# Kernel optimization log

Measured on AMD Instinct MI355X. Metric: run time of the kernel, lower is better.

The kernel has to match this reference:

```python
import jax, jax.numpy as jnp
import numpy as np

EPS = 1e-5  # BatchNorm2d default eps
HEAD_DIM = 64


def conv1x1_bn_silu(x, w, gamma, beta, mean, var):
    # x: [B, Cin, H, W], w: [Cout, Cin] (1x1 conv, no bias)
    y = jnp.einsum('oc,bchw->bohw', w, x)
    scale = (gamma / jnp.sqrt(var + EPS))[None, :, None, None]
    shift = (beta - mean * gamma / jnp.sqrt(var + EPS))[None, :, None, None]
    y = y * scale + shift
    return y * jax.nn.sigmoid(y)  # SiLU


def setup_inputs() -> dict:
    key = jax.random.key(0)
    ks = jax.random.split(key, 11)
    B, C, H, W = 4, 256, 64, 64
    C3 = 3 * C
    return {
        'x': jax.random.normal(ks[0], (B, C, H, W), jnp.float32),
        'qkv_w': jax.random.normal(ks[1], (C3, C), jnp.float32) * (1.0 / np.sqrt(C)),
        'qkv_gamma': jax.random.uniform(ks[2], (C3,), jnp.float32, 0.5, 1.5),
        'qkv_beta': jax.random.normal(ks[3], (C3,), jnp.float32) * 0.1,
        'qkv_mean': jax.random.normal(ks[4], (C3,), jnp.float32) * 0.1,
        'qkv_var': jax.random.uniform(ks[5], (C3,), jnp.float32, 0.5, 1.5),
        'proj_w': jax.random.normal(ks[6], (C, C), jnp.float32) * (1.0 / np.sqrt(C)),
        'proj_gamma': jax.random.uniform(ks[7], (C,), jnp.float32, 0.5, 1.5),
        'proj_beta': jax.random.normal(ks[8], (C,), jnp.float32) * 0.1,
        'proj_mean': jax.random.normal(ks[9], (C,), jnp.float32) * 0.1,
        'proj_var': jax.random.uniform(ks[10], (C,), jnp.float32, 0.5, 1.5),
    }


def reference(x, qkv_w, qkv_gamma, qkv_beta, qkv_mean, qkv_var,
              proj_w, proj_gamma, proj_beta, proj_mean, proj_var):
    B, C, H, W = x.shape
    hd = HEAD_DIM
    nh = C // hd
    scale = hd ** -0.5

    qkv = conv1x1_bn_silu(x, qkv_w, qkv_gamma, qkv_beta, qkv_mean, qkv_var)
    # [B, 3C, H, W] -> [B, 3, nh, hd, HW] -> (3, B, nh, HW, hd)
    qkv = qkv.reshape(B, 3, nh, hd, H * W).transpose(1, 0, 2, 4, 3)
    q, k, v = qkv[0], qkv[1], qkv[2]  # each [B, nh, HW, hd]

    attn = jnp.einsum('bhqd,bhkd->bhqk', q, k) * scale
    attn = jax.nn.softmax(attn, axis=-1)
    out = jnp.einsum('bhqk,bhkd->bhqd', attn, v)  # [B, nh, HW, hd]
    out = out.transpose(0, 1, 3, 2).reshape(B, C, H, W)

    return conv1x1_bn_silu(out, proj_w, proj_gamma, proj_beta, proj_mean, proj_var)
```

## Files before the change

kernel.cpp:

```cpp
#include <hip/hip_runtime.h>
#include <hip/hip_bf16.h>
#include <math.h>

#define SLEN 4096
#define CIN 256
#define C3 768
#define NH 4
#define HD 64
#define BATCH 4

typedef __attribute__((ext_vector_type(8))) short bf16x8;
typedef __attribute__((ext_vector_type(4))) float f32x4;
typedef __attribute__((ext_vector_type(16))) float f32x16;

typedef const __attribute__((address_space(1))) void GVoid;
typedef __attribute__((address_space(3))) void LVoid;

__device__ __forceinline__ void gl2lds16(const void* g, void* l) {
    __builtin_amdgcn_global_load_lds((GVoid*)g, (LVoid*)l, 16, 0, 0);
}

__device__ __forceinline__ short f2bf(float f) {
    union { float f; unsigned u; } v; v.f = f;
    unsigned r = v.u + 0x7fff + ((v.u >> 16) & 1);
    return (short)(r >> 16);
}

__device__ __forceinline__ unsigned cvt_pk(float lo, float hi) {
    unsigned r;
    asm("v_cvt_pk_bf16_f32 %0, %1, %2" : "=v"(r) : "v"(lo), "v"(hi));
    return r;
}

__global__ void k_convert_w(const float* __restrict__ qkvw, const float* __restrict__ projw,
                            short* __restrict__ qkvw_bf, short* __restrict__ projw_bf) {
    int i = blockIdx.x * 256 + threadIdx.x;
    if (i < C3 * CIN) qkvw_bf[i] = f2bf(qkvw[i]);
    if (i < CIN * CIN) projw_bf[i] = f2bf(projw[i]);
}

__global__ void k_transpose_x(const float* __restrict__ x, short* __restrict__ xT) {
    __shared__ float t[32][33];
    int b = blockIdx.z;
    int c0 = blockIdx.y * 32, s0 = blockIdx.x * 32;
    int tid = threadIdx.x;
    int r = tid >> 3, c4 = (tid & 7) * 4;
    const float* src = x + ((size_t)b * CIN + c0 + r) * SLEN + s0 + c4;
    float4 v = *reinterpret_cast<const float4*>(src);
    t[r][c4 + 0] = v.x; t[r][c4 + 1] = v.y; t[r][c4 + 2] = v.z; t[r][c4 + 3] = v.w;
    __syncthreads();
    int s_r = tid >> 3, cc = (tid & 7) * 4;
    short4 o = make_short4(f2bf(t[cc + 0][s_r]), f2bf(t[cc + 1][s_r]),
                           f2bf(t[cc + 2][s_r]), f2bf(t[cc + 3][s_r]));
    *reinterpret_cast<short4*>(xT + ((size_t)b * SLEN + s0 + s_r) * CIN + c0 + cc) = o;
}

__launch_bounds__(256)
__global__ void k_qkv(const short* __restrict__ xT, const short* __restrict__ wbf,
                      const float* __restrict__ g, const float* __restrict__ be,
                      const float* __restrict__ mu, const float* __restrict__ va,
                      short* __restrict__ Q, short* __restrict__ Kb, short* __restrict__ Vt) {
    int wv = threadIdx.x >> 6, l = threadIdx.x & 63, lr = l & 15, lg = l >> 4;
    int b = blockIdx.z;
    int s0 = blockIdx.x * 128 + wv * 32;
    int o0 = blockIdx.y * 64;
    f32x4 acc[2][4] = {};
    const short* aptr = xT + ((size_t)b * SLEN + s0 + lr) * CIN + lg * 8;
    const short* bptr = wbf + (size_t)(o0 + lr) * CIN + lg * 8;
#pragma unroll
    for (int k0 = 0; k0 < CIN; k0 += 32) {
        bf16x8 a0 = *(const bf16x8*)(aptr + k0);
        bf16x8 a1 = *(const bf16x8*)(aptr + 16 * CIN + k0);
#pragma unroll
        for (int oj = 0; oj < 4; oj++) {
            bf16x8 bb = *(const bf16x8*)(bptr + oj * 16 * CIN + k0);
            acc[0][oj] = __builtin_amdgcn_mfma_f32_16x16x32_bf16(a0, bb, acc[0][oj], 0, 0, 0);
            acc[1][oj] = __builtin_amdgcn_mfma_f32_16x16x32_bf16(a1, bb, acc[1][oj], 0, 0, 0);
        }
    }
    int which = o0 >> 8;
    int h = (o0 & 255) >> 6;
    int bh = b * NH + h;
    const float QSC = 0.125f * 1.44269504088896f;
#pragma unroll
    for (int oj = 0; oj < 4; oj++) {
        int o = o0 + oj * 16 + lr;
        float sc = g[o] * rsqrtf(va[o] + 1e-5f);
        float sh = be[o] - mu[o] * sc;
        int d = o & 63;
#pragma unroll
        for (int qi = 0; qi < 2; qi++) {
#pragma unroll
            for (int i = 0; i < 4; i++) {
                float y = acc[qi][oj][i] * sc + sh;
                float z = y / (1.f + __expf(-y));
                int s = s0 + qi * 16 + lg * 4 + i;
                if (which == 0) {
                    Q[((size_t)bh * SLEN + s) * HD + d] = f2bf(z * QSC);
                } else if (which == 1) {
                    Kb[((size_t)bh * SLEN + s) * HD + d] = f2bf(z);
                } else {
                    Vt[((size_t)bh * HD + d) * SLEN + s] = f2bf(z);
                }
            }
        }
    }
}

__launch_bounds__(256, 2)
__global__ void k_attn(const short* __restrict__ Q, const short* __restrict__ Kg,
                       const short* __restrict__ Vg, short* __restrict__ aout) {
    __shared__ __align__(16) char lds[16384 + 32768];
    int tid = threadIdx.x;
    int wv = tid >> 6, l = tid & 63;
    int q32 = l & 31;
    int hi  = l >> 5;

    int bid = blockIdx.x;
    int xcd = bid & 7, slot = bid >> 3;
    int bh = 2 * xcd + (slot & 1);
    int q0 = (slot >> 1) * 128 + wv * 32;

    const short* kg = Kg + (size_t)bh * SLEN * HD;
    const short* vg = Vg + (size_t)bh * HD * SLEN;

    bf16x8 qf[4];
    {
        const short* qb = Q + ((size_t)bh * SLEN + q0 + q32) * HD + hi * 8;
        qf[0] = *(const bf16x8*)(qb);
        qf[1] = *(const bf16x8*)(qb + 16);
        qf[2] = *(const bf16x8*)(qb + 32);
        qf[3] = *(const bf16x8*)(qb + 48);
    }

    bf16x8 ones;
#pragma unroll
    for (int e = 0; e < 8; ++e) ones[e] = (short)0x3F80;

    f32x16 oacc0 = {}, oacc1 = {}, sacc = {};
    float mrun = 0.0f, bA = 0.0f, bB = 0.0f;

    int colsw = (((l & 7) ^ (l >> 3)) << 4);
    const char* kgB = (const char*)kg;
    const char* vgB = (const char*)vg;
    int ksrc = (wv * 16 + (l >> 3)) * 128 + colsw;
    int vsrc = (wv * 16 + (l >> 3)) * 8192 + colsw;
    int wdst = wv * 2048;

#define STAGE(T, KB, VB) do { \
    gl2lds16(kgB + (size_t)(T) * 8192 + ksrc,          lds + (KB) * 8192 + wdst); \
    gl2lds16(kgB + (size_t)(T) * 8192 + ksrc + 1024,   lds + (KB) * 8192 + wdst + 1024); \
    gl2lds16(vgB + (size_t)(T) * 128 + vsrc,           lds + 16384 + (VB) * 8192 + wdst); \
    gl2lds16(vgB + (size_t)(T) * 128 + vsrc + 65536,   lds + 16384 + (VB) * 8192 + wdst + 1024); \
} while (0)

#define VMBAR() do { \
    asm volatile("s_waitcnt vmcnt(0) lgkmcnt(0)" ::: "memory"); \
    __builtin_amdgcn_s_barrier(); \
    asm volatile("" ::: "memory"); \
} while (0)

    int swz = (l & 7) << 4;
    int a0 = q32 * 128 + ((0 * 32 + hi * 16) ^ swz);
    int a1 = q32 * 128 + ((1 * 32 + hi * 16) ^ swz);
    int a2 = q32 * 128 + ((2 * 32 + hi * 16) ^ swz);
    int a3 = q32 * 128 + ((3 * 32 + hi * 16) ^ swz);

#define QKT(KB, D0, D1, BSET) do { \
    BSET = mrun; \
    float nb_ = -mrun; \
    _Pragma("unroll") for (int r_ = 0; r_ < 16; ++r_) { D0[r_] = nb_; D1[r_] = nb_; } \
    __builtin_amdgcn_s_setprio(1); \
    { \
        bf16x8 k0_, k1_; \
        k0_ = *(const bf16x8*)(lds + a0 + (KB) * 8192); \
        k1_ = *(const bf16x8*)(lds + a0 + (KB) * 8192 + 4096); \
        D0 = __builtin_amdgcn_mfma_f32_32x32x16_bf16(k0_, qf[0], D0, 0, 0, 0); \
        D1 = __builtin_amdgcn_mfma_f32_32x32x16_bf16(k1_, qf[0], D1, 0, 0, 0); \
        k0_ = *(const bf16x8*)(lds + a1 + (KB) * 8192); \
        k1_ = *(const bf16x8*)(lds + a1 + (KB) * 8192 + 4096); \
        D0 = __builtin_amdgcn_mfma_f32_32x32x16_bf16(k0_, qf[1], D0, 0, 0, 0); \
        D1 = __builtin_amdgcn_mfma_f32_32x32x16_bf16(k1_, qf[1], D1, 0, 0, 0); \
        k0_ = *(const bf16x8*)(lds + a2 + (KB) * 8192); \
        k1_ = *(const bf16x8*)(lds + a2 + (KB) * 8192 + 4096); \
        D0 = __builtin_amdgcn_mfma_f32_32x32x16_bf16(k0_, qf[2], D0, 0, 0, 0); \
        D1 = __builtin_amdgcn_mfma_f32_32x32x16_bf16(k1_, qf[2], D1, 0, 0, 0); \
        k0_ = *(const bf16x8*)(lds + a3 + (KB) * 8192); \
        k1_ = *(const bf16x8*)(lds + a3 + (KB) * 8192 + 4096); \
        D0 = __builtin_amdgcn_mfma_f32_32x32x16_bf16(k0_, qf[3], D0, 0, 0, 0); \
        D1 = __builtin_amdgcn_mfma_f32_32x32x16_bf16(k1_, qf[3], D1, 0, 0, 0); \
    } \
    __builtin_amdgcn_s_setprio(0); \
} while (0)

#define PVKC(AK, SV, BASE, VB) do { \
    unsigned A0_ = cvt_pk(SV[(BASE) + 0], SV[(BASE) + 1]); \
    unsigned A1_ = cvt_pk(SV[(BASE) + 2], SV[(BASE) + 3]); \
    unsigned A2_ = cvt_pk(SV[(BASE) + 4], SV[(BASE) + 5]); \
    unsigned A3_ = cvt_pk(SV[(BASE) + 6], SV[(BASE) + 7]); \
    asm volatile("v_permlane32_swap_b32 %0, %1" : "+v"(A0_), "+v"(A2_)); \
    asm volatile("v_permlane32_swap_b32 %0, %1" : "+v"(A1_), "+v"(A3_)); \
    union { bf16x8 v; unsigned u[4]; } pf_; \
    pf_.u[0] = A0_; pf_.u[1] = A1_; pf_.u[2] = A2_; pf_.u[3] = A3_; \
    bf16x8 v0_ = *(const bf16x8*)(lds + (AK) + 16384 + (VB) * 8192); \
    bf16x8 v1_ = *(const bf16x8*)(lds + (AK) + 16384 + (VB) * 8192 + 4096); \
    oacc0 = __builtin_amdgcn_mfma_f32_32x32x16_bf16(v0_, pf_.v, oacc0, 0, 0, 0); \
    oacc1 = __builtin_amdgcn_mfma_f32_32x32x16_bf16(v1_, pf_.v, oacc1, 0, 0, 0); \
    sacc  = __builtin_amdgcn_mfma_f32_32x32x16_bf16(ones, pf_.v, sacc, 0, 0, 0); \
} while (0)

#define SMPV(VB, S0, S1, BSET) do { \
    float pa_ = S0[0], pb_ = S0[8], pc_ = S1[0], pd_ = S1[8]; \
    _Pragma("unroll") for (int r_ = 1; r_ < 8; ++r_) { \
        pa_ = fmaxf(pa_, S0[r_]); pb_ = fmaxf(pb_, S0[8 + r_]); \
        pc_ = fmaxf(pc_, S1[r_]); pd_ = fmaxf(pd_, S1[8 + r_]); \
    } \
    float pms_ = fmaxf(fmaxf(pa_, pb_), fmaxf(pc_, pd_)); \
    float c1_ = pms_, c2_ = pms_; \
    asm volatile("" : "+v"(c2_));  \
    asm volatile("v_permlane32_swap_b32 %0, %1" : "+v"(c1_), "+v"(c2_)); \
    pms_ = fmaxf(c1_, c2_); \
    float db_ = mrun - (BSET); \
    if (!__all(pms_ <= db_ + 10.0f)) { \
        float mn_ = fmaxf(mrun, pms_ + (BSET)); \
        float al_ = __builtin_amdgcn_exp2f(mrun - mn_); \
        _Pragma("unroll") for (int r_ = 0; r_ < 16; ++r_) { oacc0[r_] *= al_; oacc1[r_] *= al_; } \
        sacc[0] *= al_; \
        mrun = mn_; db_ = mn_ - (BSET); \
    } \
    if (__all(db_ == 0.0f)) { \
        _Pragma("unroll") for (int r_ = 0; r_ < 16; ++r_) { \
            S0[r_] = __builtin_amdgcn_exp2f(S0[r_]); \
            S1[r_] = __builtin_amdgcn_exp2f(S1[r_]); \
        } \
    } else { \
        _Pragma("unroll") for (int r_ = 0; r_ < 16; ++r_) { \
            S0[r_] = __builtin_amdgcn_exp2f(S0[r_] - db_); \
            S1[r_] = __builtin_amdgcn_exp2f(S1[r_] - db_); \
        } \
    } \
    __builtin_amdgcn_s_setprio(1); \
    PVKC(a0, S0, 0, VB); \
    PVKC(a1, S0, 8, VB); \
    PVKC(a2, S1, 0, VB); \
    PVKC(a3, S1, 8, VB); \
    __builtin_amdgcn_s_setprio(0); \
} while (0)

    f32x16 sA0, sA1, sB0, sB1;

    STAGE(0, 0, 0);
    VMBAR();
    STAGE(1, 1, 1);
    QKT(0, sA0, sA1, bA);
    VMBAR();

    for (int j = 0; j < 15; ++j) {
        STAGE(4 * j + 2, 0, 2); QKT(1, sB0, sB1, bB); SMPV(0, sA0, sA1, bA); VMBAR();
        STAGE(4 * j + 3, 1, 3); QKT(0, sA0, sA1, bA); SMPV(1, sB0, sB1, bB); VMBAR();
        STAGE(4 * j + 4, 0, 0); QKT(1, sB0, sB1, bB); SMPV(2, sA0, sA1, bA); VMBAR();
        STAGE(4 * j + 5, 1, 1); QKT(0, sA0, sA1, bA); SMPV(3, sB0, sB1, bB); VMBAR();
    }
    STAGE(62, 0, 2); QKT(1, sB0, sB1, bB); SMPV(0, sA0, sA1, bA); VMBAR();
    STAGE(63, 1, 3); QKT(0, sA0, sA1, bA); SMPV(1, sB0, sB1, bB); VMBAR();
    QKT(1, sB0, sB1, bB); SMPV(2, sA0, sA1, bA);
    SMPV(3, sB0, sB1, bB);

    float inv = 1.f / sacc[0];
    int b = bh >> 2, h = bh & 3;
    short* ob = aout + ((size_t)b * SLEN + q0 + q32) * CIN + h * HD;
#pragma unroll
    for (int g4 = 0; g4 < 4; ++g4) {
        uint2 st0, st1;
        st0.x = cvt_pk(oacc0[4 * g4 + 0] * inv, oacc0[4 * g4 + 1] * inv);
        st0.y = cvt_pk(oacc0[4 * g4 + 2] * inv, oacc0[4 * g4 + 3] * inv);
        st1.x = cvt_pk(oacc1[4 * g4 + 0] * inv, oacc1[4 * g4 + 1] * inv);
        st1.y = cvt_pk(oacc1[4 * g4 + 2] * inv, oacc1[4 * g4 + 3] * inv);
        *(uint2*)(ob + 8 * g4 + 4 * hi) = st0;
        *(uint2*)(ob + 32 + 8 * g4 + 4 * hi) = st1;
    }
#undef STAGE
#undef VMBAR
#undef QKT
#undef PVKC
#undef SMPV
}

__launch_bounds__(256)
__global__ void k_proj(const short* __restrict__ aout, const short* __restrict__ wbf,
                       const float* __restrict__ g, const float* __restrict__ be,
                       const float* __restrict__ mu, const float* __restrict__ va,
                       float* __restrict__ out) {
    int wv = threadIdx.x >> 6, l = threadIdx.x & 63, lr = l & 15, lg = l >> 4;
    int b = blockIdx.z;
    int s0 = blockIdx.x * 128 + wv * 32;
    int o0 = blockIdx.y * 64;
    f32x4 acc[2][4] = {};
    const short* aptr = aout + ((size_t)b * SLEN + s0 + lr) * CIN + lg * 8;
    const short* bptr = wbf + (size_t)(o0 + lr) * CIN + lg * 8;
#pragma unroll
    for (int k0 = 0; k0 < CIN; k0 += 32) {
        bf16x8 a0 = *(const bf16x8*)(aptr + k0);
        bf16x8 a1 = *(const bf16x8*)(aptr + 16 * CIN + k0);
#pragma unroll
        for (int oj = 0; oj < 4; oj++) {
            bf16x8 bb = *(const bf16x8*)(bptr + oj * 16 * CIN + k0);
            acc[0][oj] = __builtin_amdgcn_mfma_f32_16x16x32_bf16(a0, bb, acc[0][oj], 0, 0, 0);
            acc[1][oj] = __builtin_amdgcn_mfma_f32_16x16x32_bf16(a1, bb, acc[1][oj], 0, 0, 0);
        }
    }
#pragma unroll
    for (int oj = 0; oj < 4; oj++) {
        int o = o0 + oj * 16 + lr;
        float sc = g[o] * rsqrtf(va[o] + 1e-5f);
        float sh = be[o] - mu[o] * sc;
#pragma unroll
        for (int qi = 0; qi < 2; qi++) {
            float4 st;
            float* stp = &st.x;
#pragma unroll
            for (int i = 0; i < 4; i++) {
                float y = acc[qi][oj][i] * sc + sh;
                stp[i] = y / (1.f + __expf(-y));
            }
            int s = s0 + qi * 16 + lg * 4;
            *reinterpret_cast<float4*>(out + ((size_t)b * CIN + o) * SLEN + s) = st;
        }
    }
}

extern "C" void kernel_launch(void* const* d_in, const int* in_sizes, int n_in,
                              void* d_out, int out_size, void* d_ws, size_t ws_size,
                              hipStream_t stream) {
    const float* x    = (const float*)d_in[0];
    const float* qkvw = (const float*)d_in[1];
    const float* qg   = (const float*)d_in[2];
    const float* qbe  = (const float*)d_in[3];
    const float* qmu  = (const float*)d_in[4];
    const float* qva  = (const float*)d_in[5];
    const float* pw   = (const float*)d_in[6];
    const float* pg   = (const float*)d_in[7];
    const float* pbe  = (const float*)d_in[8];
    const float* pmu  = (const float*)d_in[9];
    const float* pva  = (const float*)d_in[10];
    float* out = (float*)d_out;

    char* ws = (char*)d_ws;
    short* xT       = (short*)(ws);
    short* qkvw_bf  = (short*)(ws + 8388608);
    short* projw_bf = (short*)(ws + 8781824);
    short* Qb       = (short*)(ws + 8912896);
    short* Kb       = (short*)(ws + 17301504);
    short* Vt       = (short*)(ws + 25690112);
    short* aout     = (short*)(ws + 34078720);

    k_convert_w<<<768, 256, 0, stream>>>(qkvw, pw, qkvw_bf, projw_bf);
    k_transpose_x<<<dim3(128, 8, 4), 256, 0, stream>>>(x, xT);
    k_qkv<<<dim3(32, 12, 4), 256, 0, stream>>>(xT, qkvw_bf, qg, qbe, qmu, qva, Qb, Kb, Vt);
    k_attn<<<512, 256, 0, stream>>>(Qb, Kb, Vt, aout);
    k_proj<<<dim3(32, 4, 4), 256, 0, stream>>>(aout, projw_bf, pg, pbe, pmu, pva, out);
}
```

Measured before the change: 159.7 us.

## Process two 32-row query tiles per wave to reuse K/V LDS loads

```diff
diff --git a/kernel.cpp b/kernel.cpp
--- a/kernel.cpp
+++ b/kernel.cpp
@@ -107,7 +107,7 @@
     }
 }
 
-__launch_bounds__(256, 2)
+__launch_bounds__(256, 1)
 __global__ void k_attn(const short* __restrict__ Q, const short* __restrict__ Kg,
                        const short* __restrict__ Vg, short* __restrict__ aout) {
     __shared__ __align__(16) char lds[16384 + 32768];
@@ -119,26 +119,31 @@
     int bid = blockIdx.x;
     int xcd = bid & 7, slot = bid >> 3;
     int bh = 2 * xcd + (slot & 1);
-    int q0 = (slot >> 1) * 128 + wv * 32;
+    int q0 = (slot >> 1) * 256 + wv * 64;
 
     const short* kg = Kg + (size_t)bh * SLEN * HD;
     const short* vg = Vg + (size_t)bh * HD * SLEN;
 
-    bf16x8 qf[4];
+    bf16x8 qfL[4], qfR[4];
     {
         const short* qb = Q + ((size_t)bh * SLEN + q0 + q32) * HD + hi * 8;
-        qf[0] = *(const bf16x8*)(qb);
-        qf[1] = *(const bf16x8*)(qb + 16);
-        qf[2] = *(const bf16x8*)(qb + 32);
-        qf[3] = *(const bf16x8*)(qb + 48);
+        qfL[0] = *(const bf16x8*)(qb);
+        qfL[1] = *(const bf16x8*)(qb + 16);
+        qfL[2] = *(const bf16x8*)(qb + 32);
+        qfL[3] = *(const bf16x8*)(qb + 48);
+        const short* qb2 = qb + 32 * HD;
+        qfR[0] = *(const bf16x8*)(qb2);
+        qfR[1] = *(const bf16x8*)(qb2 + 16);
+        qfR[2] = *(const bf16x8*)(qb2 + 32);
+        qfR[3] = *(const bf16x8*)(qb2 + 48);
     }
 
     bf16x8 ones;
 #pragma unroll
     for (int e = 0; e < 8; ++e) ones[e] = (short)0x3F80;
 
-    f32x16 oacc0 = {}, oacc1 = {}, sacc = {};
-    float mrun = 0.0f, bA = 0.0f, bB = 0.0f;
+    f32x16 oaccL0 = {}, oaccL1 = {}, oaccR0 = {}, oaccR1 = {}, saccL = {}, saccR = {};
+    float mrunL = 0.0f, mrunR = 0.0f, bAL = 0.0f, bAR = 0.0f, bBL = 0.0f, bBR = 0.0f;
 
     int colsw = (((l & 7) ^ (l >> 3)) << 4);
     const char* kgB = (const char*)kg;
@@ -166,124 +171,158 @@
     int a2 = q32 * 128 + ((2 * 32 + hi * 16) ^ swz);
     int a3 = q32 * 128 + ((3 * 32 + hi * 16) ^ swz);
 
-#define QKT(KB, D0, D1, BSET) do { \
-    BSET = mrun; \
-    float nb_ = -mrun; \
-    _Pragma("unroll") for (int r_ = 0; r_ < 16; ++r_) { D0[r_] = nb_; D1[r_] = nb_; } \
+#define MM(A, B, C) __builtin_amdgcn_mfma_f32_32x32x16_bf16(A, B, C, 0, 0, 0)
+
+#define QKT2(KB, DL0, DL1, DR0, DR1, BL, BR) do { \
+    BL = mrunL; BR = mrunR; \
+    float nbl_ = -mrunL, nbr_ = -mrunR; \
+    _Pragma("unroll") for (int r_ = 0; r_ < 16; ++r_) { \
+        DL0[r_] = nbl_; DL1[r_] = nbl_; DR0[r_] = nbr_; DR1[r_] = nbr_; } \
     __builtin_amdgcn_s_setprio(1); \
     { \
         bf16x8 k0_, k1_; \
         k0_ = *(const bf16x8*)(lds + a0 + (KB) * 8192); \
         k1_ = *(const bf16x8*)(lds + a0 + (KB) * 8192 + 4096); \
-        D0 = __builtin_amdgcn_mfma_f32_32x32x16_bf16(k0_, qf[0], D0, 0, 0, 0); \
-        D1 = __builtin_amdgcn_mfma_f32_32x32x16_bf16(k1_, qf[0], D1, 0, 0, 0); \
+        DL0 = MM(k0_, qfL[0], DL0); DL1 = MM(k1_, qfL[0], DL1); \
+        DR0 = MM(k0_, qfR[0], DR0); DR1 = MM(k1_, qfR[0], DR1); \
         k0_ = *(const bf16x8*)(lds + a1 + (KB) * 8192); \
         k1_ = *(const bf16x8*)(lds + a1 + (KB) * 8192 + 4096); \
-        D0 = __builtin_amdgcn_mfma_f32_32x32x16_bf16(k0_, qf[1], D0, 0, 0, 0); \
-        D1 = __builtin_amdgcn_mfma_f32_32x32x16_bf16(k1_, qf[1], D1, 0, 0, 0); \
+        DL0 = MM(k0_, qfL[1], DL0); DL1 = MM(k1_, qfL[1], DL1); \
+        DR0 = MM(k0_, qfR[1], DR0); DR1 = MM(k1_, qfR[1], DR1); \
         k0_ = *(const bf16x8*)(lds + a2 + (KB) * 8192); \
         k1_ = *(const bf16x8*)(lds + a2 + (KB) * 8192 + 4096); \
-        D0 = __builtin_amdgcn_mfma_f32_32x32x16_bf16(k0_, qf[2], D0, 0, 0, 0); \
-        D1 = __builtin_amdgcn_mfma_f32_32x32x16_bf16(k1_, qf[2], D1, 0, 0, 0); \
+        DL0 = MM(k0_, qfL[2], DL0); DL1 = MM(k1_, qfL[2], DL1); \
+        DR0 = MM(k0_, qfR[2], DR0); DR1 = MM(k1_, qfR[2], DR1); \
         k0_ = *(const bf16x8*)(lds + a3 + (KB) * 8192); \
         k1_ = *(const bf16x8*)(lds + a3 + (KB) * 8192 + 4096); \
-        D0 = __builtin_amdgcn_mfma_f32_32x32x16_bf16(k0_, qf[3], D0, 0, 0, 0); \
-        D1 = __builtin_amdgcn_mfma_f32_32x32x16_bf16(k1_, qf[3], D1, 0, 0, 0); \
+        DL0 = MM(k0_, qfL[3], DL0); DL1 = MM(k1_, qfL[3], DL1); \
+        DR0 = MM(k0_, qfR[3], DR0); DR1 = MM(k1_, qfR[3], DR1); \
     } \
     __builtin_amdgcn_s_setprio(0); \
 } while (0)
 
-#define PVKC(AK, SV, BASE, VB) do { \
-    unsigned A0_ = cvt_pk(SV[(BASE) + 0], SV[(BASE) + 1]); \
-    unsigned A1_ = cvt_pk(SV[(BASE) + 2], SV[(BASE) + 3]); \
-    unsigned A2_ = cvt_pk(SV[(BASE) + 4], SV[(BASE) + 5]); \
-    unsigned A3_ = cvt_pk(SV[(BASE) + 6], SV[(BASE) + 7]); \
-    asm volatile("v_permlane32_swap_b32 %0, %1" : "+v"(A0_), "+v"(A2_)); \
-    asm volatile("v_permlane32_swap_b32 %0, %1" : "+v"(A1_), "+v"(A3_)); \
-    union { bf16x8 v; unsigned u[4]; } pf_; \
-    pf_.u[0] = A0_; pf_.u[1] = A1_; pf_.u[2] = A2_; pf_.u[3] = A3_; \
+#define PVKC2(AK, SL, SR, BASE, VB) do { \
+    unsigned L0_ = cvt_pk(SL[(BASE) + 0], SL[(BASE) + 1]); \
+    unsigned L1_ = cvt_pk(SL[(BASE) + 2], SL[(BASE) + 3]); \
+    unsigned L2_ = cvt_pk(SL[(BASE) + 4], SL[(BASE) + 5]); \
+    unsigned L3_ = cvt_pk(SL[(BASE) + 6], SL[(BASE) + 7]); \
+    asm volatile("v_permlane32_swap_b32 %0, %1" : "+v"(L0_), "+v"(L2_)); \
+    asm volatile("v_permlane32_swap_b32 %0, %1" : "+v"(L1_), "+v"(L3_)); \
+    unsigned R0_ = cvt_pk(SR[(BASE) + 0], SR[(BASE) + 1]); \
+    unsigned R1_ = cvt_pk(SR[(BASE) + 2], SR[(BASE) + 3]); \
+    unsigned R2_ = cvt_pk(SR[(BASE) + 4], SR[(BASE) + 5]); \
+    unsigned R3_ = cvt_pk(SR[(BASE) + 6], SR[(BASE) + 7]); \
+    asm volatile("v_permlane32_swap_b32 %0, %1" : "+v"(R0_), "+v"(R2_)); \
+    asm volatile("v_permlane32_swap_b32 %0, %1" : "+v"(R1_), "+v"(R3_)); \
+    union { bf16x8 v; unsigned u[4]; } pfL_, pfR_; \
+    pfL_.u[0] = L0_; pfL_.u[1] = L1_; pfL_.u[2] = L2_; pfL_.u[3] = L3_; \
+    pfR_.u[0] = R0_; pfR_.u[1] = R1_; pfR_.u[2] = R2_; pfR_.u[3] = R3_; \
     bf16x8 v0_ = *(const bf16x8*)(lds + (AK) + 16384 + (VB) * 8192); \
     bf16x8 v1_ = *(const bf16x8*)(lds + (AK) + 16384 + (VB) * 8192 + 4096); \
-    oacc0 = __builtin_amdgcn_mfma_f32_32x32x16_bf16(v0_, pf_.v, oacc0, 0, 0, 0); \
-    oacc1 = __builtin_amdgcn_mfma_f32_32x32x16_bf16(v1_, pf_.v, oacc1, 0, 0, 0); \
-    sacc  = __builtin_amdgcn_mfma_f32_32x32x16_bf16(ones, pf_.v, sacc, 0, 0, 0); \
+    oaccL0 = MM(v0_, pfL_.v, oaccL0); oaccL1 = MM(v1_, pfL_.v, oaccL1); \
+    oaccR0 = MM(v0_, pfR_.v, oaccR0); oaccR1 = MM(v1_, pfR_.v, oaccR1); \
+    saccL = MM(ones, pfL_.v, saccL);  saccR = MM(ones, pfR_.v, saccR); \
 } while (0)
 
-#define SMPV(VB, S0, S1, BSET) do { \
-    float pa_ = S0[0], pb_ = S0[8], pc_ = S1[0], pd_ = S1[8]; \
+#define SMPV2(VB, SL0, SL1, SR0, SR1, BL, BR) do { \
+    float paL_ = SL0[0], pbL_ = SL0[8], pcL_ = SL1[0], pdL_ = SL1[8]; \
+    float paR_ = SR0[0], pbR_ = SR0[8], pcR_ = SR1[0], pdR_ = SR1[8]; \
     _Pragma("unroll") for (int r_ = 1; r_ < 8; ++r_) { \
-        pa_ = fmaxf(pa_, S0[r_]); pb_ = fmaxf(pb_, S0[8 + r_]); \
-        pc_ = fmaxf(pc_, S1[r_]); pd_ = fmaxf(pd_, S1[8 + r_]); \
+        paL_ = fmaxf(paL_, SL0[r_]); pbL_ = fmaxf(pbL_, SL0[8 + r_]); \
+        pcL_ = fmaxf(pcL_, SL1[r_]); pdL_ = fmaxf(pdL_, SL1[8 + r_]); \
+        paR_ = fmaxf(paR_, SR0[r_]); pbR_ = fmaxf(pbR_, SR0[8 + r_]); \
+        pcR_ = fmaxf(pcR_, SR1[r_]); pdR_ = fmaxf(pdR_, SR1[8 + r_]); \
     } \
-    float pms_ = fmaxf(fmaxf(pa_, pb_), fmaxf(pc_, pd_)); \
-    float c1_ = pms_, c2_ = pms_; \
-    asm volatile("" : "+v"(c2_));  \
-    asm volatile("v_permlane32_swap_b32 %0, %1" : "+v"(c1_), "+v"(c2_)); \
-    pms_ = fmaxf(c1_, c2_); \
-    float db_ = mrun - (BSET); \
-    if (!__all(pms_ <= db_ + 10.0f)) { \
-        float mn_ = fmaxf(mrun, pms_ + (BSET)); \
-        float al_ = __builtin_amdgcn_exp2f(mrun - mn_); \
-        _Pragma("unroll") for (int r_ = 0; r_ < 16; ++r_) { oacc0[r_] *= al_; oacc1[r_] *= al_; } \
-        sacc[0] *= al_; \
-        mrun = mn_; db_ = mn_ - (BSET); \
+    float pmsL_ = fmaxf(fmaxf(paL_, pbL_), fmaxf(pcL_, pdL_)); \
+    float pmsR_ = fmaxf(fmaxf(paR_, pbR_), fmaxf(pcR_, pdR_)); \
+    { float c1_ = pmsL_, c2_ = pmsL_; \
+      asm volatile("" : "+v"(c2_)); \
+      asm volatile("v_permlane32_swap_b32 %0, %1" : "+v"(c1_), "+v"(c2_)); \
+      pmsL_ = fmaxf(c1_, c2_); } \
+    { float c1_ = pmsR_, c2_ = pmsR_; \
+      asm volatile("" : "+v"(c2_)); \
+      asm volatile("v_permlane32_swap_b32 %0, %1" : "+v"(c1_), "+v"(c2_)); \
+      pmsR_ = fmaxf(c1_, c2_); } \
+    float dbL_ = mrunL - (BL), dbR_ = mrunR - (BR); \
+    if (!__all((pmsL_ <= dbL_ + 10.0f) && (pmsR_ <= dbR_ + 10.0f))) { \
+        float mnL_ = fmaxf(mrunL, pmsL_ + (BL)); \
+        float alL_ = __builtin_amdgcn_exp2f(mrunL - mnL_); \
+        float mnR_ = fmaxf(mrunR, pmsR_ + (BR)); \
+        float alR_ = __builtin_amdgcn_exp2f(mrunR - mnR_); \
+        _Pragma("unroll") for (int r_ = 0; r_ < 16; ++r_) { \
+            oaccL0[r_] *= alL_; oaccL1[r_] *= alL_; \
+            oaccR0[r_] *= alR_; oaccR1[r_] *= alR_; } \
+        saccL[0] *= alL_; saccR[0] *= alR_; \
+        mrunL = mnL_; dbL_ = mnL_ - (BL); \
+        mrunR = mnR_; dbR_ = mnR_ - (BR); \
     } \
-    if (__all(db_ == 0.0f)) { \
+    if (__all((dbL_ == 0.0f) && (dbR_ == 0.0f))) { \
         _Pragma("unroll") for (int r_ = 0; r_ < 16; ++r_) { \
-            S0[r_] = __builtin_amdgcn_exp2f(S0[r_]); \
-            S1[r_] = __builtin_amdgcn_exp2f(S1[r_]); \
-        } \
+            SL0[r_] = __builtin_amdgcn_exp2f(SL0[r_]); \
+            SL1[r_] = __builtin_amdgcn_exp2f(SL1[r_]); \
+            SR0[r_] = __builtin_amdgcn_exp2f(SR0[r_]); \
+            SR1[r_] = __builtin_amdgcn_exp2f(SR1[r_]); } \
     } else { \
         _Pragma("unroll") for (int r_ = 0; r_ < 16; ++r_) { \
-            S0[r_] = __builtin_amdgcn_exp2f(S0[r_] - db_); \
-            S1[r_] = __builtin_amdgcn_exp2f(S1[r_] - db_); \
-        } \
+            SL0[r_] = __builtin_amdgcn_exp2f(SL0[r_] - dbL_); \
+            SL1[r_] = __builtin_amdgcn_exp2f(SL1[r_] - dbL_); \
+            SR0[r_] = __builtin_amdgcn_exp2f(SR0[r_] - dbR_); \
+            SR1[r_] = __builtin_amdgcn_exp2f(SR1[r_] - dbR_); } \
     } \
     __builtin_amdgcn_s_setprio(1); \
-    PVKC(a0, S0, 0, VB); \
-    PVKC(a1, S0, 8, VB); \
-    PVKC(a2, S1, 0, VB); \
-    PVKC(a3, S1, 8, VB); \
+    PVKC2(a0, SL0, SR0, 0, VB); \
+    PVKC2(a1, SL0, SR0, 8, VB); \
+    PVKC2(a2, SL1, SR1, 0, VB); \
+    PVKC2(a3, SL1, SR1, 8, VB); \
     __builtin_amdgcn_s_setprio(0); \
 } while (0)
 
-    f32x16 sA0, sA1, sB0, sB1;
+    f32x16 sAL0, sAL1, sAR0, sAR1, sBL0, sBL1, sBR0, sBR1;
 
     STAGE(0, 0, 0);
     VMBAR();
     STAGE(1, 1, 1);
-    QKT(0, sA0, sA1, bA);
+    QKT2(0, sAL0, sAL1, sAR0, sAR1, bAL, bAR);
     VMBAR();
 
     for (int j = 0; j < 15; ++j) {
-        STAGE(4 * j + 2, 0, 2); QKT(1, sB0, sB1, bB); SMPV(0, sA0, sA1, bA); VMBAR();
-        STAGE(4 * j + 3, 1, 3); QKT(0, sA0, sA1, bA); SMPV(1, sB0, sB1, bB); VMBAR();
-        STAGE(4 * j + 4, 0, 0); QKT(1, sB0, sB1, bB); SMPV(2, sA0, sA1, bA); VMBAR();
-        STAGE(4 * j + 5, 1, 1); QKT(0, sA0, sA1, bA); SMPV(3, sB0, sB1, bB); VMBAR();
-    }
-    STAGE(62, 0, 2); QKT(1, sB0, sB1, bB); SMPV(0, sA0, sA1, bA); VMBAR();
-    STAGE(63, 1, 3); QKT(0, sA0, sA1, bA); SMPV(1, sB0, sB1, bB); VMBAR();
-    QKT(1, sB0, sB1, bB); SMPV(2, sA0, sA1, bA);
-    SMPV(3, sB0, sB1, bB);
-
-    float inv = 1.f / sacc[0];
+        STAGE(4 * j + 2, 0, 2); QKT2(1, sBL0, sBL1, sBR0, sBR1, bBL, bBR); SMPV2(0, sAL0, sAL1, sAR0, sAR1, bAL, bAR); VMBAR();
+        STAGE(4 * j + 3, 1, 3); QKT2(0, sAL0, sAL1, sAR0, sAR1, bAL, bAR); SMPV2(1, sBL0, sBL1, sBR0, sBR1, bBL, bBR); VMBAR();
+        STAGE(4 * j + 4, 0, 0); QKT2(1, sBL0, sBL1, sBR0, sBR1, bBL, bBR); SMPV2(2, sAL0, sAL1, sAR0, sAR1, bAL, bAR); VMBAR();
+        STAGE(4 * j + 5, 1, 1); QKT2(0, sAL0, sAL1, sAR0, sAR1, bAL, bAR); SMPV2(3, sBL0, sBL1, sBR0, sBR1, bBL, bBR); VMBAR();
+    }
+    STAGE(62, 0, 2); QKT2(1, sBL0, sBL1, sBR0, sBR1, bBL, bBR); SMPV2(0, sAL0, sAL1, sAR0, sAR1, bAL, bAR); VMBAR();
+    STAGE(63, 1, 3); QKT2(0, sAL0, sAL1, sAR0, sAR1, bAL, bAR); SMPV2(1, sBL0, sBL1, sBR0, sBR1, bBL, bBR); VMBAR();
+    QKT2(1, sBL0, sBL1, sBR0, sBR1, bBL, bBR); SMPV2(2, sAL0, sAL1, sAR0, sAR1, bAL, bAR);
+    SMPV2(3, sBL0, sBL1, sBR0, sBR1, bBL, bBR);
+
+    float invL = 1.f / saccL[0];
+    float invR = 1.f / saccR[0];
     int b = bh >> 2, h = bh & 3;
-    short* ob = aout + ((size_t)b * SLEN + q0 + q32) * CIN + h * HD;
+    short* obL = aout + ((size_t)b * SLEN + q0 + q32) * CIN + h * HD;
+    short* obR = obL + 32 * CIN;
 #pragma unroll
     for (int g4 = 0; g4 < 4; ++g4) {
         uint2 st0, st1;
-        st0.x = cvt_pk(oacc0[4 * g4 + 0] * inv, oacc0[4 * g4 + 1] * inv);
-        st0.y = cvt_pk(oacc0[4 * g4 + 2] * inv, oacc0[4 * g4 + 3] * inv);
-        st1.x = cvt_pk(oacc1[4 * g4 + 0] * inv, oacc1[4 * g4 + 1] * inv);
-        st1.y = cvt_pk(oacc1[4 * g4 + 2] * inv, oacc1[4 * g4 + 3] * inv);
-        *(uint2*)(ob + 8 * g4 + 4 * hi) = st0;
-        *(uint2*)(ob + 32 + 8 * g4 + 4 * hi) = st1;
+        st0.x = cvt_pk(oaccL0[4 * g4 + 0] * invL, oaccL0[4 * g4 + 1] * invL);
+        st0.y = cvt_pk(oaccL0[4 * g4 + 2] * invL, oaccL0[4 * g4 + 3] * invL);
+        st1.x = cvt_pk(oaccL1[4 * g4 + 0] * invL, oaccL1[4 * g4 + 1] * invL);
+        st1.y = cvt_pk(oaccL1[4 * g4 + 2] * invL, oaccL1[4 * g4 + 3] * invL);
+        *(uint2*)(obL + 8 * g4 + 4 * hi) = st0;
+        *(uint2*)(obL + 32 + 8 * g4 + 4 * hi) = st1;
+        st0.x = cvt_pk(oaccR0[4 * g4 + 0] * invR, oaccR0[4 * g4 + 1] * invR);
+        st0.y = cvt_pk(oaccR0[4 * g4 + 2] * invR, oaccR0[4 * g4 + 3] * invR);
+        st1.x = cvt_pk(oaccR1[4 * g4 + 0] * invR, oaccR1[4 * g4 + 1] * invR);
+        st1.y = cvt_pk(oaccR1[4 * g4 + 2] * invR, oaccR1[4 * g4 + 3] * invR);
+        *(uint2*)(obR + 8 * g4 + 4 * hi) = st0;
+        *(uint2*)(obR + 32 + 8 * g4 + 4 * hi) = st1;
     }
 #undef STAGE
 #undef VMBAR
-#undef QKT
-#undef PVKC
-#undef SMPV
+#undef MM
+#undef QKT2
+#undef PVKC2
+#undef SMPV2
 }
 
 __launch_bounds__(256)
@@ -357,6 +396,6 @@
     k_convert_w<<<768, 256, 0, stream>>>(qkvw, pw, qkvw_bf, projw_bf);
     k_transpose_x<<<dim3(128, 8, 4), 256, 0, stream>>>(x, xT);
     k_qkv<<<dim3(32, 12, 4), 256, 0, stream>>>(xT, qkvw_bf, qg, qbe, qmu, qva, Qb, Kb, Vt);
-    k_attn<<<512, 256, 0, stream>>>(Qb, Kb, Vt, aout);
+    k_attn<<<256, 256, 0, stream>>>(Qb, Kb, Vt, aout);
     k_proj<<<dim3(32, 4, 4), 256, 0, stream>>>(aout, projw_bf, pg, pbe, pmu, pva, out);
 }
```

Result: slower. 166.8 us (+4.5%).

## Restructure attention pipeline to two-tile stages and compute softmax sum on VALU

Applied to the files above, without the earlier changes.

```diff
diff --git a/kernel.cpp b/kernel.cpp
--- a/kernel.cpp
+++ b/kernel.cpp
@@ -110,7 +110,7 @@
 __launch_bounds__(256, 2)
 __global__ void k_attn(const short* __restrict__ Q, const short* __restrict__ Kg,
                        const short* __restrict__ Vg, short* __restrict__ aout) {
-    __shared__ __align__(16) char lds[16384 + 32768];
+    __shared__ __align__(16) char lds[32768 + 32768];
     int tid = threadIdx.x;
     int wv = tid >> 6, l = tid & 63;
     int q32 = l & 31;
@@ -133,12 +133,8 @@
         qf[3] = *(const bf16x8*)(qb + 48);
     }
 
-    bf16x8 ones;
-#pragma unroll
-    for (int e = 0; e < 8; ++e) ones[e] = (short)0x3F80;
-
-    f32x16 oacc0 = {}, oacc1 = {}, sacc = {};
-    float mrun = 0.0f, bA = 0.0f, bB = 0.0f;
+    f32x16 oacc0 = {}, oacc1 = {};
+    float mrun = 0.0f, bA = 0.0f, bB = 0.0f, srun = 0.0f;
 
     int colsw = (((l & 7) ^ (l >> 3)) << 4);
     const char* kgB = (const char*)kg;
@@ -150,12 +146,12 @@
 #define STAGE(T, KB, VB) do { \
     gl2lds16(kgB + (size_t)(T) * 8192 + ksrc,          lds + (KB) * 8192 + wdst); \
     gl2lds16(kgB + (size_t)(T) * 8192 + ksrc + 1024,   lds + (KB) * 8192 + wdst + 1024); \
-    gl2lds16(vgB + (size_t)(T) * 128 + vsrc,           lds + 16384 + (VB) * 8192 + wdst); \
-    gl2lds16(vgB + (size_t)(T) * 128 + vsrc + 65536,   lds + 16384 + (VB) * 8192 + wdst + 1024); \
+    gl2lds16(vgB + (size_t)(T) * 128 + vsrc,           lds + 32768 + (VB) * 8192 + wdst); \
+    gl2lds16(vgB + (size_t)(T) * 128 + vsrc + 65536,   lds + 32768 + (VB) * 8192 + wdst + 1024); \
 } while (0)
 
 #define VMBAR() do { \
-    asm volatile("s_waitcnt vmcnt(0) lgkmcnt(0)" ::: "memory"); \
+    asm volatile("s_waitcnt vmcnt(0)" ::: "memory"); \
     __builtin_amdgcn_s_barrier(); \
     asm volatile("" ::: "memory"); \
 } while (0)
@@ -202,11 +198,10 @@
     asm volatile("v_permlane32_swap_b32 %0, %1" : "+v"(A1_), "+v"(A3_)); \
     union { bf16x8 v; unsigned u[4]; } pf_; \
     pf_.u[0] = A0_; pf_.u[1] = A1_; pf_.u[2] = A2_; pf_.u[3] = A3_; \
-    bf16x8 v0_ = *(const bf16x8*)(lds + (AK) + 16384 + (VB) * 8192); \
-    bf16x8 v1_ = *(const bf16x8*)(lds + (AK) + 16384 + (VB) * 8192 + 4096); \
+    bf16x8 v0_ = *(const bf16x8*)(lds + (AK) + 32768 + (VB) * 8192); \
+    bf16x8 v1_ = *(const bf16x8*)(lds + (AK) + 32768 + (VB) * 8192 + 4096); \
     oacc0 = __builtin_amdgcn_mfma_f32_32x32x16_bf16(v0_, pf_.v, oacc0, 0, 0, 0); \
     oacc1 = __builtin_amdgcn_mfma_f32_32x32x16_bf16(v1_, pf_.v, oacc1, 0, 0, 0); \
-    sacc  = __builtin_amdgcn_mfma_f32_32x32x16_bf16(ones, pf_.v, sacc, 0, 0, 0); \
 } while (0)
 
 #define SMPV(VB, S0, S1, BSET) do { \
@@ -225,7 +220,7 @@
         float mn_ = fmaxf(mrun, pms_ + (BSET)); \
         float al_ = __builtin_amdgcn_exp2f(mrun - mn_); \
         _Pragma("unroll") for (int r_ = 0; r_ < 16; ++r_) { oacc0[r_] *= al_; oacc1[r_] *= al_; } \
-        sacc[0] *= al_; \
+        srun *= al_; \
         mrun = mn_; db_ = mn_ - (BSET); \
     } \
     if (__all(db_ == 0.0f)) { \
@@ -239,6 +234,13 @@
             S1[r_] = __builtin_amdgcn_exp2f(S1[r_] - db_); \
         } \
     } \
+    { \
+        float t0_ = 0.f, t1_ = 0.f, t2_ = 0.f, t3_ = 0.f; \
+        _Pragma("unroll") for (int r_ = 0; r_ < 8; ++r_) { \
+            t0_ += S0[r_]; t1_ += S0[8 + r_]; t2_ += S1[r_]; t3_ += S1[8 + r_]; \
+        } \
+        srun += (t0_ + t1_) + (t2_ + t3_); \
+    } \
     __builtin_amdgcn_s_setprio(1); \
     PVKC(a0, S0, 0, VB); \
     PVKC(a1, S0, 8, VB); \
@@ -250,23 +252,31 @@
     f32x16 sA0, sA1, sB0, sB1;
 
     STAGE(0, 0, 0);
+    STAGE(1, 1, 1);
     VMBAR();
-    STAGE(1, 1, 1);
-    QKT(0, sA0, sA1, bA);
+
+    for (int m = 0; m < 15; ++m) {
+        int t = 4 * m;
+        STAGE(t + 2, 2, 2); STAGE(t + 3, 3, 3);
+        QKT(0, sA0, sA1, bA); QKT(1, sB0, sB1, bB);
+        SMPV(0, sA0, sA1, bA); SMPV(1, sB0, sB1, bB);
+        VMBAR();
+        STAGE(t + 4, 0, 0); STAGE(t + 5, 1, 1);
+        QKT(2, sA0, sA1, bA); QKT(3, sB0, sB1, bB);
+        SMPV(2, sA0, sA1, bA); SMPV(3, sB0, sB1, bB);
+        VMBAR();
+    }
+    STAGE(62, 2, 2); STAGE(63, 3, 3);
+    QKT(0, sA0, sA1, bA); QKT(1, sB0, sB1, bB);
+    SMPV(0, sA0, sA1, bA); SMPV(1, sB0, sB1, bB);
     VMBAR();
-
-    for (int j = 0; j < 15; ++j) {
-        STAGE(4 * j + 2, 0, 2); QKT(1, sB0, sB1, bB); SMPV(0, sA0, sA1, bA); VMBAR();
-        STAGE(4 * j + 3, 1, 3); QKT(0, sA0, sA1, bA); SMPV(1, sB0, sB1, bB); VMBAR();
-        STAGE(4 * j + 4, 0, 0); QKT(1, sB0, sB1, bB); SMPV(2, sA0, sA1, bA); VMBAR();
-        STAGE(4 * j + 5, 1, 1); QKT(0, sA0, sA1, bA); SMPV(3, sB0, sB1, bB); VMBAR();
-    }
-    STAGE(62, 0, 2); QKT(1, sB0, sB1, bB); SMPV(0, sA0, sA1, bA); VMBAR();
-    STAGE(63, 1, 3); QKT(0, sA0, sA1, bA); SMPV(1, sB0, sB1, bB); VMBAR();
-    QKT(1, sB0, sB1, bB); SMPV(2, sA0, sA1, bA);
-    SMPV(3, sB0, sB1, bB);
-
-    float inv = 1.f / sacc[0];
+    QKT(2, sA0, sA1, bA); QKT(3, sB0, sB1, bB);
+    SMPV(2, sA0, sA1, bA); SMPV(3, sB0, sB1, bB);
+
+    float c1 = srun, c2 = srun;
+    asm volatile("" : "+v"(c2));
+    asm volatile("v_permlane32_swap_b32 %0, %1" : "+v"(c1), "+v"(c2));
+    float inv = 1.f / (c1 + c2);
     int b = bh >> 2, h = bh & 3;
     short* ob = aout + ((size_t)b * SLEN + q0 + q32) * CIN + h * HD;
 #pragma unroll
```

Result: no change. 160.2 us (+0.3%).
